# Optimization experiments

Measured on AMD Instinct MI355X. Metric: run time of the kernel, lower is better.

Reference implementation:

```python
import jax, jax.numpy as jnp
import numpy as np

N = 100000      # nodes
E = 1600000     # edges (avg degree 16)
G = 2000        # graphs
D_IN = 4        # node_in_dim
H = 128         # hidden_dim
L = 3           # num_layers


def setup_inputs() -> dict:
    key = jax.random.key(0)
    ks = jax.random.split(key, 16)
    si = 1.0 / np.sqrt(D_IN)
    sh = 1.0 / np.sqrt(H)
    inp = {
        "x": jax.random.normal(ks[0], (N, D_IN), jnp.float32),
        "edge_index": jax.random.randint(ks[1], (2, E), 0, N, dtype=jnp.int32),
        "batch": jnp.sort(jax.random.randint(ks[2], (N,), 0, G, dtype=jnp.int32)),
        "proj_w": jax.random.normal(ks[3], (D_IN, H), jnp.float32) * si,
        "proj_b": jnp.zeros((H,), jnp.float32),
        "conv_w1": jax.random.normal(ks[4], (L, H, H), jnp.float32) * sh,
        "conv_b1": jnp.zeros((L, H), jnp.float32),
        "conv_w2": jax.random.normal(ks[5], (L, H, H), jnp.float32) * sh,
        "conv_b2": jnp.zeros((L, H), jnp.float32),
        "shared_w": jax.random.normal(ks[6], (H, H), jnp.float32) * sh,
        "shared_b": jnp.zeros((H,), jnp.float32),
        "e_w": jax.random.normal(ks[7], (H, 1), jnp.float32) * sh,
        "e_b": jnp.zeros((1,), jnp.float32),
        "d_w": jax.random.normal(ks[8], (H, 1), jnp.float32) * sh,
        "d_b": jnp.zeros((1,), jnp.float32),
    }
    return inp


def reference(x, edge_index, batch, proj_w, proj_b, conv_w1, conv_b1,
              conv_w2, conv_b2, shared_w, shared_b, e_w, e_b, d_w, d_b):
    src, dst = edge_index[0], edge_index[1]
    # input projection: [N, D_IN] -> [N, H]
    h = x @ proj_w + proj_b
    # GIN layers: h' = relu(MLP((1+eps)*h + sum_{j->i} h_j)), eps = 0
    for l in range(L):
        agg = jax.ops.segment_sum(h[src], dst, num_segments=N)  # scatter-add
        m = h + agg
        m = jax.nn.relu(m @ conv_w1[l] + conv_b1[l]) @ conv_w2[l] + conv_b2[l]
        h = jax.nn.relu(m)
    # global mean pool over graphs: [N, H] -> [G, H]
    sums = jax.ops.segment_sum(h, batch, num_segments=G)
    cnt = jax.ops.segment_sum(jnp.ones((N,), h.dtype), batch, num_segments=G)
    g = sums / jnp.maximum(cnt, 1.0)[:, None]
    # shared head (dropout inactive in eval)
    g = jax.nn.relu(g @ shared_w + shared_b)
    energy = (g @ e_w + e_b).reshape(-1)
    dipole = (g @ d_w + d_b).reshape(-1)
    return (energy, dipole)
```

## Files before the change

kernel.cpp:

```cpp
#include <hip/hip_runtime.h>
#include <hip/hip_bf16.h>

#define H 128
#define REGSZ 512
#define PCHUNK 4096

typedef short short8 __attribute__((ext_vector_type(8)));
typedef float f32x4 __attribute__((ext_vector_type(4)));

__device__ __forceinline__ float bf2f(unsigned short u) {
    union { unsigned int i; float f; } c; c.i = ((unsigned int)u) << 16; return c.f;
}
__device__ __forceinline__ unsigned short f2bf(float f) {
    return __builtin_bit_cast(unsigned short, __float2bfloat16(f));
}
__device__ __forceinline__ uint2 pack_fp8x8(const float* f) {
    unsigned int lo = 0, hi = 0;
    lo = __builtin_amdgcn_cvt_pk_fp8_f32(f[0], f[1], lo, 0);
    lo = __builtin_amdgcn_cvt_pk_fp8_f32(f[2], f[3], lo, 1);
    hi = __builtin_amdgcn_cvt_pk_fp8_f32(f[4], f[5], hi, 0);
    hi = __builtin_amdgcn_cvt_pk_fp8_f32(f[6], f[7], hi, 1);
    return make_uint2(lo, hi);
}
__device__ __forceinline__ void unpack_fp8x8(uint2 v, float* f) {
    f[0] = __builtin_amdgcn_cvt_f32_fp8(v.x, 0);
    f[1] = __builtin_amdgcn_cvt_f32_fp8(v.x, 1);
    f[2] = __builtin_amdgcn_cvt_f32_fp8(v.x, 2);
    f[3] = __builtin_amdgcn_cvt_f32_fp8(v.x, 3);
    f[4] = __builtin_amdgcn_cvt_f32_fp8(v.y, 0);
    f[5] = __builtin_amdgcn_cvt_f32_fp8(v.y, 1);
    f[6] = __builtin_amdgcn_cvt_f32_fp8(v.y, 2);
    f[7] = __builtin_amdgcn_cvt_f32_fp8(v.y, 3);
}

__global__ void prep_w_kernel(const float* __restrict__ cw1, const float* __restrict__ cw2,
                              unsigned short* __restrict__ wt, int total) {
    int idx = blockIdx.x * 256 + threadIdx.x;
    if (idx >= total) return;
    int m = idx >> 14;
    int o = (idx >> 7) & 127;
    int i = idx & 127;
    const float* srcp = (m < 3) ? (cw1 + (size_t)m * H * H) : (cw2 + (size_t)(m - 3) * H * H);
    wt[idx] = f2bf(srcp[i * H + o]);
}

__global__ void proj_kernel(const float* __restrict__ x, const float* __restrict__ pw,
                            const float* __restrict__ pb, unsigned char* __restrict__ h8, int N) {
    int tid = blockIdx.x * 256 + threadIdx.x;
    if (tid >= N * 16) return;
    int i = tid >> 4, c = (tid & 15) * 8;
    float4 xv = *(const float4*)&x[i * 4];
    float acc[8];
#pragma unroll
    for (int j = 0; j < 8; ++j)
        acc[j] = pb[c + j] + xv.x * pw[0 * H + c + j] + xv.y * pw[1 * H + c + j]
               + xv.z * pw[2 * H + c + j] + xv.w * pw[3 * H + c + j];
    *(uint2*)&h8[(size_t)i * H + c] = pack_fp8x8(acc);
}

__global__ __launch_bounds__(256) void partition_kernel(
    const int* __restrict__ src, const int* __restrict__ dst,
    int* __restrict__ rcnt, int* __restrict__ bucket,
    int E, int nreg, int cap) {
    __shared__ int hcnt[256];
    __shared__ int hbase[256];
    int tid = threadIdx.x;
    hcnt[tid] = 0;
    __syncthreads();
    int e0 = blockIdx.x * PCHUNK;
    int e1 = min(e0 + PCHUNK, E);
    for (int e = e0 + tid; e < e1; e += 256)
        atomicAdd(&hcnt[dst[e] >> 9], 1);
    __syncthreads();
    {
        int c = hcnt[tid];
        hbase[tid] = (c > 0) ? atomicAdd(&rcnt[tid], c) : 0;
        hcnt[tid] = 0;
    }
    __syncthreads();
    for (int e = e0 + tid; e < e1; e += 256) {
        int d = dst[e], s = src[e];
        int r = d >> 9;
        int pos = hbase[r] + atomicAdd(&hcnt[r], 1);
        if (pos < cap) bucket[(size_t)r * cap + pos] = ((d & (REGSZ - 1)) << 17) | s;
    }
}

__global__ __launch_bounds__(256) void csr_region_kernel(
    const int* __restrict__ rcnt, const int* __restrict__ bucket,
    int* __restrict__ offs, int* __restrict__ esrc,
    int N, int nreg, int cap) {
    __shared__ int cnt[REGSZ];
    __shared__ int part[256];
    __shared__ int sbase;
    int r = blockIdx.x;
    int tid = threadIdx.x;

    int v = (tid < nreg) ? rcnt[tid] : 0;
    part[tid] = v;
    __syncthreads();
    for (int off = 1; off < 256; off <<= 1) {
        int t = (tid >= off) ? part[tid - off] : 0;
        __syncthreads();
        part[tid] += t;
        __syncthreads();
    }
    if (tid == 0) sbase = (r == 0) ? 0 : part[r - 1];
    cnt[tid] = 0;
    cnt[tid + 256] = 0;
    __syncthreads();
    int base = sbase;
    int n = min(part[r] - base, cap);
    const int* bk = bucket + (size_t)r * cap;

    for (int p = tid; p < n; p += 256)
        atomicAdd(&cnt[bk[p] >> 17], 1);
    __syncthreads();

    int c0 = cnt[tid * 2], c1 = cnt[tid * 2 + 1];
    part[tid] = c0 + c1;
    __syncthreads();
    for (int off = 1; off < 256; off <<= 1) {
        int t = (tid >= off) ? part[tid - off] : 0;
        __syncthreads();
        part[tid] += t;
        __syncthreads();
    }
    int excl = (tid == 0) ? 0 : part[tid - 1];
    cnt[tid * 2] = excl;
    cnt[tid * 2 + 1] = excl + c0;
    __syncthreads();

    for (int p = tid; p < n; p += 256) {
        int e = bk[p];
        int pos = atomicAdd(&cnt[e >> 17], 1);
        esrc[base + pos] = e & 0x1FFFF;
    }
    __syncthreads();

    int lo = r * REGSZ;
#pragma unroll
    for (int i = tid; i < REGSZ; i += 256) {
        int node = lo + i;
        if (node < N) offs[node] = base + cnt[i];
    }
}

__global__ void gather_agg_kernel(const int* __restrict__ offs, const int* __restrict__ esrc,
                                  const unsigned char* __restrict__ h8, unsigned short* __restrict__ pre, int N) {
    int tid = blockIdx.x * 256 + threadIdx.x;
    if (tid >= N * 16) return;
    int node = tid >> 4, c = (tid & 15) * 8;
    int s = (node == 0) ? 0 : offs[node - 1];
    int e = offs[node];
    float acc[8];
    unpack_fp8x8(*(const uint2*)&h8[(size_t)node * H + c], acc);
    int i = s;
    for (; i + 3 < e; i += 4) {
        uint2 v[4];
#pragma unroll
        for (int k = 0; k < 4; ++k) v[k] = *(const uint2*)&h8[(size_t)esrc[i + k] * H + c];
#pragma unroll
        for (int k = 0; k < 4; ++k) {
            acc[0] += __builtin_amdgcn_cvt_f32_fp8(v[k].x, 0);
            acc[1] += __builtin_amdgcn_cvt_f32_fp8(v[k].x, 1);
            acc[2] += __builtin_amdgcn_cvt_f32_fp8(v[k].x, 2);
            acc[3] += __builtin_amdgcn_cvt_f32_fp8(v[k].x, 3);
            acc[4] += __builtin_amdgcn_cvt_f32_fp8(v[k].y, 0);
            acc[5] += __builtin_amdgcn_cvt_f32_fp8(v[k].y, 1);
            acc[6] += __builtin_amdgcn_cvt_f32_fp8(v[k].y, 2);
            acc[7] += __builtin_amdgcn_cvt_f32_fp8(v[k].y, 3);
        }
    }
    for (; i < e; ++i) {
        uint2 v = *(const uint2*)&h8[(size_t)esrc[i] * H + c];
        acc[0] += __builtin_amdgcn_cvt_f32_fp8(v.x, 0);
        acc[1] += __builtin_amdgcn_cvt_f32_fp8(v.x, 1);
        acc[2] += __builtin_amdgcn_cvt_f32_fp8(v.x, 2);
        acc[3] += __builtin_amdgcn_cvt_f32_fp8(v.x, 3);
        acc[4] += __builtin_amdgcn_cvt_f32_fp8(v.y, 0);
        acc[5] += __builtin_amdgcn_cvt_f32_fp8(v.y, 1);
        acc[6] += __builtin_amdgcn_cvt_f32_fp8(v.y, 2);
        acc[7] += __builtin_amdgcn_cvt_f32_fp8(v.y, 3);
    }
    short8 o;
#pragma unroll
    for (int j = 0; j < 8; ++j) o[j] = (short)f2bf(acc[j]);
    *(short8*)&pre[(size_t)node * H + c] = o;
}

template <bool LAST>
__global__ __launch_bounds__(512) void fused_mlp_kernel(
    const unsigned short* __restrict__ pre,
    const unsigned short* __restrict__ W1t, const unsigned short* __restrict__ W2t,
    const float* __restrict__ b1, const float* __restrict__ b2,
    unsigned short* __restrict__ C, unsigned char* __restrict__ h8, int N) {
    __shared__ unsigned short As[128 * H];
    __shared__ unsigned short Ws1[H * H];
    __shared__ unsigned short Ws2[H * H];
    int bm = blockIdx.x * 128;
    int tid = threadIdx.x;

#pragma unroll
    for (int rep = 0; rep < 4; ++rep) {
        int lin = rep * 512 + tid;
        int r = lin >> 4, cb = lin & 15;
        int row = bm + r;
        short8 vv = {};
        if (row < N) vv = *(const short8*)&pre[(size_t)row * H + cb * 8];
        int byte = r * 256 + ((cb * 16) ^ ((r & 7) << 4));
        *(short8*)((char*)As + byte) = vv;
    }
#pragma unroll
    for (int rep = 0; rep < 4; ++rep) {
        int lin = rep * 512 + tid;
        int o = lin >> 4, cb = lin & 15;
        int byte = o * 256 + ((cb * 16) ^ ((o & 7) << 4));
        *(short8*)((char*)Ws1 + byte) = *(const short8*)&W1t[(size_t)o * H + cb * 8];
        *(short8*)((char*)Ws2 + byte) = *(const short8*)&W2t[(size_t)o * H + cb * 8];
    }
    __syncthreads();

    int lane = tid & 63;
    int w = tid >> 6;
    int wr = (w >> 1) * 32;
    int wc = (w & 1) * 64;
    int lrow = lane & 15, kg = lane >> 4;

    float b1v[4], b2v[4];
#pragma unroll
    for (int ct = 0; ct < 4; ++ct) {
        b1v[ct] = b1[wc + ct * 16 + lrow];
        b2v[ct] = b2[wc + ct * 16 + lrow];
    }

    short8 a[2][4];
#pragma unroll
    for (int rt = 0; rt < 2; ++rt)
#pragma unroll
        for (int ks = 0; ks < 4; ++ks) {
            int r = wr + rt * 16 + lrow;
            int kb = ks * 64 + kg * 16;
            a[rt][ks] = *(short8*)((char*)As + r * 256 + (kb ^ ((r & 7) << 4)));
        }

    f32x4 acc[2][4] = {};
#pragma unroll
    for (int ct = 0; ct < 4; ++ct) {
#pragma unroll
        for (int ks = 0; ks < 4; ++ks) {
            int o = wc + ct * 16 + lrow;
            int kb = ks * 64 + kg * 16;
            short8 b = *(short8*)((char*)Ws1 + o * 256 + (kb ^ ((o & 7) << 4)));
            acc[0][ct] = __builtin_amdgcn_mfma_f32_16x16x32_bf16(a[0][ks], b, acc[0][ct], 0, 0, 0);
            acc[1][ct] = __builtin_amdgcn_mfma_f32_16x16x32_bf16(a[1][ks], b, acc[1][ct], 0, 0, 0);
        }
    }
    __syncthreads();

#pragma unroll
    for (int rt = 0; rt < 2; ++rt)
#pragma unroll
        for (int ct = 0; ct < 4; ++ct)
#pragma unroll
            for (int rr = 0; rr < 4; ++rr) {
                int r = wr + rt * 16 + kg * 4 + rr;
                int col = wc + ct * 16 + lrow;
                float v = fmaxf(acc[rt][ct][rr] + b1v[ct], 0.f);
                int byte = r * 256 + ((col * 2) ^ ((r & 7) << 4));
                *(unsigned short*)((char*)As + byte) = f2bf(v);
            }
    __syncthreads();

#pragma unroll
    for (int rt = 0; rt < 2; ++rt)
#pragma unroll
        for (int ks = 0; ks < 4; ++ks) {
            int r = wr + rt * 16 + lrow;
            int kb = ks * 64 + kg * 16;
            a[rt][ks] = *(short8*)((char*)As + r * 256 + (kb ^ ((r & 7) << 4)));
        }

    f32x4 acc2[2][4] = {};
#pragma unroll
    for (int ct = 0; ct < 4; ++ct) {
#pragma unroll
        for (int ks = 0; ks < 4; ++ks) {
            int o = wc + ct * 16 + lrow;
            int kb = ks * 64 + kg * 16;
            short8 b = *(short8*)((char*)Ws2 + o * 256 + (kb ^ ((o & 7) << 4)));
            acc2[0][ct] = __builtin_amdgcn_mfma_f32_16x16x32_bf16(a[0][ks], b, acc2[0][ct], 0, 0, 0);
            acc2[1][ct] = __builtin_amdgcn_mfma_f32_16x16x32_bf16(a[1][ks], b, acc2[1][ct], 0, 0, 0);
        }
    }
    __syncthreads();

#pragma unroll
    for (int rt = 0; rt < 2; ++rt)
#pragma unroll
        for (int ct = 0; ct < 4; ++ct)
#pragma unroll
            for (int rr = 0; rr < 4; ++rr) {
                int r = wr + rt * 16 + kg * 4 + rr;
                int col = wc + ct * 16 + lrow;
                float v = fmaxf(acc2[rt][ct][rr] + b2v[ct], 0.f);
                As[r * H + col] = f2bf(v);
            }
    __syncthreads();

#pragma unroll
    for (int rep = 0; rep < 4; ++rep) {
        int lin = rep * 512 + tid;
        int r = lin >> 4, cb = lin & 15;
        int row = bm + r;
        if (row < N) {
            short8 v = *(short8*)&As[r * H + cb * 8];
            if (LAST) {
                *(short8*)&C[(size_t)row * H + cb * 8] = v;
            } else {
                float f[8];
#pragma unroll
                for (int j = 0; j < 8; ++j) f[j] = bf2f((unsigned short)v[j]);
                *(uint2*)&h8[(size_t)row * H + cb * 8] = pack_fp8x8(f);
            }
        }
    }
}

__global__ __launch_bounds__(128) void pool_head_kernel(
    const unsigned short* __restrict__ h, const int* __restrict__ batch,
    const float* __restrict__ sw, const float* __restrict__ sb,
    const float* __restrict__ ew, const float* __restrict__ eb,
    const float* __restrict__ dw, const float* __restrict__ db,
    float* __restrict__ out, int N, int G) {
    int g = blockIdx.x;
    int j = threadIdx.x;
    int s, e;
    {
        int lo = 0, hi = N;
        while (lo < hi) { int mid = (lo + hi) >> 1; if (batch[mid] < g) lo = mid + 1; else hi = mid; }
        s = lo;
        hi = N;
        while (lo < hi) { int mid = (lo + hi) >> 1; if (batch[mid] < g + 1) lo = mid + 1; else hi = mid; }
        e = lo;
    }
    float sum = 0.f;
    for (int n = s; n < e; ++n) sum += bf2f(h[(size_t)n * H + j]);
    float cnt = (float)(e - s);
    __shared__ float gm[H];
    gm[j] = sum / fmaxf(cnt, 1.0f);
    __syncthreads();
    float t = sb[j];
    for (int k = 0; k < H; ++k) t += gm[k] * sw[k * H + j];
    t = fmaxf(t, 0.f);
    __shared__ float red[2][H];
    red[0][j] = t * ew[j];
    red[1][j] = t * dw[j];
    __syncthreads();
    for (int off = 64; off > 0; off >>= 1) {
        if (j < off) {
            red[0][j] += red[0][j + off];
            red[1][j] += red[1][j + off];
        }
        __syncthreads();
    }
    if (j == 0) {
        out[g] = red[0][0] + eb[0];
        out[G + g] = red[1][0] + db[0];
    }
}

extern "C" void kernel_launch(void* const* d_in, const int* in_sizes, int n_in,
                              void* d_out, int out_size, void* d_ws, size_t ws_size,
                              hipStream_t stream) {
    const float* x      = (const float*)d_in[0];
    const int*   ei     = (const int*)d_in[1];
    const int*   batch  = (const int*)d_in[2];
    const float* proj_w = (const float*)d_in[3];
    const float* proj_b = (const float*)d_in[4];
    const float* cw1    = (const float*)d_in[5];
    const float* cb1    = (const float*)d_in[6];
    const float* cw2    = (const float*)d_in[7];
    const float* cb2    = (const float*)d_in[8];
    const float* sw     = (const float*)d_in[9];
    const float* sb     = (const float*)d_in[10];
    const float* ew     = (const float*)d_in[11];
    const float* eb     = (const float*)d_in[12];
    const float* dw     = (const float*)d_in[13];
    const float* db     = (const float*)d_in[14];

    int N = in_sizes[0] / 4;
    int E = in_sizes[1] / 2;
    int G = out_size / 2;

    const int* src = ei;
    const int* dst = ei + E;

    unsigned short* h   = (unsigned short*)d_ws;
    unsigned short* pre = h + (size_t)N * H;
    unsigned short* wt  = pre + (size_t)N * H;
    int* offs  = (int*)(wt + 6 * H * H);
    int* rcnt  = offs + N + 1;
    int* esrc  = rcnt + 256;
    unsigned char* h8 = (unsigned char*)(esrc + E);
    int* bucket = (int*)pre;

    float* out = (float*)d_out;

    int nreg = (N + REGSZ - 1) >> 9;
    int cap  = (E / nreg) * 5 / 4 + 1024;

    hipMemsetAsync(rcnt, 0, 256 * sizeof(int), stream);

    partition_kernel<<<(E + PCHUNK - 1) / PCHUNK, 256, 0, stream>>>(src, dst, rcnt, bucket, E, nreg, cap);
    csr_region_kernel<<<nreg, 256, 0, stream>>>(rcnt, bucket, offs, esrc, N, nreg, cap);

    prep_w_kernel<<<(6 * H * H + 255) / 256, 256, 0, stream>>>(cw1, cw2, wt, 6 * H * H);
    proj_kernel<<<(N * 16 + 255) / 256, 256, 0, stream>>>(x, proj_w, proj_b, h8, N);

    int mlp_blocks = (N + 127) / 128;
    int gather_blocks = (N * 16 + 255) / 256;

    for (int l = 0; l < 3; ++l) {
        gather_agg_kernel<<<gather_blocks, 256, 0, stream>>>(offs, esrc, h8, pre, N);
        if (l < 2)
            fused_mlp_kernel<false><<<mlp_blocks, 512, 0, stream>>>(
                pre, wt + (size_t)l * H * H, wt + (size_t)(3 + l) * H * H,
                cb1 + l * H, cb2 + l * H, h, h8, N);
        else
            fused_mlp_kernel<true><<<mlp_blocks, 512, 0, stream>>>(
                pre, wt + (size_t)l * H * H, wt + (size_t)(3 + l) * H * H,
                cb1 + l * H, cb2 + l * H, h, h8, N);
    }

    pool_head_kernel<<<G, 128, 0, stream>>>(h, batch, sw, sb, ew, eb, dw, db, out, N, G);
}
```

Baseline: 326.8 us.

## Fuse global mean-pool sums into last MLP layer via atomics

The last fused MLP layer now accumulates per-graph column sums straight from shared memory into a zeroed gsum buffer with atomicAdd, run-length merging the sorted batch ids. This removes writing the final bf16 hidden state to global memory and the pool kernel's serial per-graph read of it. The head kernel then only divides by counts and applies the MLPs. Float atomics make the summation order nondeterministic, and the memset grows to cover the gsum buffer.

```diff
diff --git a/kernel.cpp b/kernel.cpp
--- a/kernel.cpp
+++ b/kernel.cpp
@@ -194,10 +194,12 @@
     const unsigned short* __restrict__ pre,
     const unsigned short* __restrict__ W1t, const unsigned short* __restrict__ W2t,
     const float* __restrict__ b1, const float* __restrict__ b2,
-    unsigned short* __restrict__ C, unsigned char* __restrict__ h8, int N) {
+    unsigned char* __restrict__ h8, const int* __restrict__ batch,
+    float* __restrict__ gsum, int N) {
     __shared__ unsigned short As[128 * H];
     __shared__ unsigned short Ws1[H * H];
     __shared__ unsigned short Ws2[H * H];
+    __shared__ int sbatch[128];
     int bm = blockIdx.x * 128;
     int tid = threadIdx.x;
 
@@ -219,6 +221,10 @@
         *(short8*)((char*)Ws1 + byte) = *(const short8*)&W1t[(size_t)o * H + cb * 8];
         *(short8*)((char*)Ws2 + byte) = *(const short8*)&W2t[(size_t)o * H + cb * 8];
     }
+    if (LAST && tid < 128) {
+        int row = bm + tid;
+        sbatch[tid] = (row < N) ? batch[row] : -1;
+    }
     __syncthreads();
 
     int lane = tid & 63;
@@ -308,27 +314,42 @@
             }
     __syncthreads();
 
-#pragma unroll
-    for (int rep = 0; rep < 4; ++rep) {
-        int lin = rep * 512 + tid;
-        int r = lin >> 4, cb = lin & 15;
-        int row = bm + r;
-        if (row < N) {
-            short8 v = *(short8*)&As[r * H + cb * 8];
-            if (LAST) {
-                *(short8*)&C[(size_t)row * H + cb * 8] = v;
-            } else {
+    if (!LAST) {
+#pragma unroll
+        for (int rep = 0; rep < 4; ++rep) {
+            int lin = rep * 512 + tid;
+            int r = lin >> 4, cb = lin & 15;
+            int row = bm + r;
+            if (row < N) {
+                short8 v = *(short8*)&As[r * H + cb * 8];
                 float f[8];
 #pragma unroll
                 for (int j = 0; j < 8; ++j) f[j] = bf2f((unsigned short)v[j]);
                 *(uint2*)&h8[(size_t)row * H + cb * 8] = pack_fp8x8(f);
             }
         }
-    }
-}
-
-__global__ __launch_bounds__(128) void pool_head_kernel(
-    const unsigned short* __restrict__ h, const int* __restrict__ batch,
+    } else {
+        if (tid < 128) {
+            int col = tid;
+            int rmax = min(128, N - bm);
+            float acc = 0.f;
+            int cur = sbatch[0];
+            for (int r = 0; r < rmax; ++r) {
+                int g = sbatch[r];
+                if (g != cur) {
+                    atomicAdd(&gsum[(size_t)cur * H + col], acc);
+                    cur = g;
+                    acc = 0.f;
+                }
+                acc += bf2f(As[r * H + col]);
+            }
+            if (rmax > 0) atomicAdd(&gsum[(size_t)cur * H + col], acc);
+        }
+    }
+}
+
+__global__ __launch_bounds__(128) void head_kernel(
+    const float* __restrict__ gsum, const int* __restrict__ batch,
     const float* __restrict__ sw, const float* __restrict__ sb,
     const float* __restrict__ ew, const float* __restrict__ eb,
     const float* __restrict__ dw, const float* __restrict__ db,
@@ -344,11 +365,9 @@
         while (lo < hi) { int mid = (lo + hi) >> 1; if (batch[mid] < g + 1) lo = mid + 1; else hi = mid; }
         e = lo;
     }
-    float sum = 0.f;
-    for (int n = s; n < e; ++n) sum += bf2f(h[(size_t)n * H + j]);
     float cnt = (float)(e - s);
     __shared__ float gm[H];
-    gm[j] = sum / fmaxf(cnt, 1.0f);
+    gm[j] = gsum[(size_t)g * H + j] / fmaxf(cnt, 1.0f);
     __syncthreads();
     float t = sb[j];
     for (int k = 0; k < H; ++k) t += gm[k] * sw[k * H + j];
@@ -396,12 +415,12 @@
     const int* src = ei;
     const int* dst = ei + E;
 
-    unsigned short* h   = (unsigned short*)d_ws;
-    unsigned short* pre = h + (size_t)N * H;
+    unsigned short* pre = (unsigned short*)d_ws;
     unsigned short* wt  = pre + (size_t)N * H;
     int* offs  = (int*)(wt + 6 * H * H);
     int* rcnt  = offs + N + 1;
-    int* esrc  = rcnt + 256;
+    float* gsum = (float*)(rcnt + 256);
+    int* esrc  = (int*)(gsum + (size_t)G * H);
     unsigned char* h8 = (unsigned char*)(esrc + E);
     int* bucket = (int*)pre;
 
@@ -410,7 +429,7 @@
     int nreg = (N + REGSZ - 1) >> 9;
     int cap  = (E / nreg) * 5 / 4 + 1024;
 
-    hipMemsetAsync(rcnt, 0, 256 * sizeof(int), stream);
+    hipMemsetAsync(rcnt, 0, (256 + (size_t)G * H) * sizeof(int), stream);
 
     partition_kernel<<<(E + PCHUNK - 1) / PCHUNK, 256, 0, stream>>>(src, dst, rcnt, bucket, E, nreg, cap);
     csr_region_kernel<<<nreg, 256, 0, stream>>>(rcnt, bucket, offs, esrc, N, nreg, cap);
@@ -426,12 +445,12 @@
         if (l < 2)
             fused_mlp_kernel<false><<<mlp_blocks, 512, 0, stream>>>(
                 pre, wt + (size_t)l * H * H, wt + (size_t)(3 + l) * H * H,
-                cb1 + l * H, cb2 + l * H, h, h8, N);
+                cb1 + l * H, cb2 + l * H, h8, batch, gsum, N);
         else
             fused_mlp_kernel<true><<<mlp_blocks, 512, 0, stream>>>(
                 pre, wt + (size_t)l * H * H, wt + (size_t)(3 + l) * H * H,
-                cb1 + l * H, cb2 + l * H, h, h8, N);
-    }
-
-    pool_head_kernel<<<G, 128, 0, stream>>>(h, batch, sw, sb, ew, eb, dw, db, out, N, G);
-}
+                cb1 + l * H, cb2 + l * H, h8, batch, gsum, N);
+    }
+
+    head_kernel<<<G, 128, 0, stream>>>(gsum, batch, sw, sb, ew, eb, dw, db, out, N, G);
+}
```

Result: slower. 340.4 us (+4.2%).
